# Optimization experiments

Measured on AMD Instinct MI355X. Metric: run time of the kernel, lower is better.

The kernel has to match this reference:

```python
import jax, jax.numpy as jnp
import numpy as np

CODEBOOK = 512
EMB_DIM = 64
COMMITMENT_COST = 0.25


def setup_inputs() -> dict:
    key = jax.random.key(0)
    k1, k2 = jax.random.split(key)
    inputs = jax.random.normal(k1, (32, EMB_DIM, 64, 64), dtype=jnp.float32)
    # nn.Embedding weight initialized uniform(-1/code_book_dim, 1/code_book_dim)
    embedding = jax.random.uniform(
        k2, (CODEBOOK, EMB_DIM), dtype=jnp.float32,
        minval=-1.0 / CODEBOOK, maxval=1.0 / CODEBOOK)
    return {"inputs": inputs, "embedding": embedding}


def reference(inputs, embedding):
    B, C, H, W = inputs.shape          # C == embedding_dim
    D = embedding.shape[1]
    x = jnp.transpose(inputs, (0, 2, 3, 1))      # [B,H,W,D] (permute(0,2,3,1))
    flat = x.reshape(-1, D)                       # [N,D]
    x2 = jnp.sum(flat * flat, axis=1, keepdims=True)          # [N,1]
    e2 = jnp.sum(embedding * embedding, axis=1)[None, :]       # [1,K]
    xe = flat @ embedding.T                                    # [N,K]
    distances = (x2 - 2.0 * xe + e2) / D                       # [N,K]
    encoding_indices = jnp.argmin(distances, axis=1)           # [N]
    quantized = embedding[encoding_indices].reshape(x.shape)   # [B,H,W,D]
    # MSE losses with detach semantics
    e_latent_loss = jnp.mean((jax.lax.stop_gradient(quantized) - x) ** 2)
    q_latent_loss = jnp.mean((quantized - jax.lax.stop_gradient(x)) ** 2)
    loss = q_latent_loss + COMMITMENT_COST * e_latent_loss
    # straight-through estimator (module default training=True)
    quantized_st = x + jax.lax.stop_gradient(quantized - x)
    out = jnp.transpose(quantized_st, (0, 3, 1, 2))            # back to NCHW
    indices = encoding_indices.reshape(B, -1)                  # [B, H*W]
    return loss, out, indices
```

## Files before the change

kernel.cpp:

```cpp
#include <hip/hip_runtime.h>


#define KCODE 512
#define EMB   64
#define HWSZ  4096
#define NPOS  131072
#define DELTA 2.5e-4f

typedef short short8  __attribute__((ext_vector_type(8)));
typedef float float4v __attribute__((ext_vector_type(4)));


__device__ __forceinline__ float np_sumsq64(const float* a) {
    #pragma clang fp contract(off)
    {
        float r0 = a[0] * a[0], r1 = a[1] * a[1], r2 = a[2] * a[2], r3 = a[3] * a[3];
        float r4 = a[4] * a[4], r5 = a[5] * a[5], r6 = a[6] * a[6], r7 = a[7] * a[7];
        for (int i = 8; i < 64; i += 8) {
            r0 += a[i + 0] * a[i + 0];
            r1 += a[i + 1] * a[i + 1];
            r2 += a[i + 2] * a[i + 2];
            r3 += a[i + 3] * a[i + 3];
            r4 += a[i + 4] * a[i + 4];
            r5 += a[i + 5] * a[i + 5];
            r6 += a[i + 6] * a[i + 6];
            r7 += a[i + 7] * a[i + 7];
        }
        return ((r0 + r1) + (r2 + r3)) + ((r4 + r5) + (r6 + r7));
    }
}

__device__ __forceinline__ float exact_u(const float* x, float x2,
                                         const float* ek, float e2k) {
    float t0 = 0.f, t1 = 0.f, t2 = 0.f, t3 = 0.f;
    #pragma unroll
    for (int c = 0; c < EMB; c += 4) {
        t0 = fmaf(x[c + 0], ek[c + 0], t0);
        t1 = fmaf(x[c + 1], ek[c + 1], t1);
        t2 = fmaf(x[c + 2], ek[c + 2], t2);
        t3 = fmaf(x[c + 3], ek[c + 3], t3);
    }
    float xe  = (t0 + t1) + (t2 + t3);
    float tmp = x2 - 2.0f * xe;
    return tmp + e2k;
}

__device__ __forceinline__ unsigned short bf16rne(float f) {
    unsigned u = __float_as_uint(f);
    unsigned r = (u + 0x7FFFu + ((u >> 16) & 1u)) >> 16;
    return (unsigned short)r;
}
__device__ __forceinline__ float bf16tof(unsigned short h) {
    return __uint_as_float((unsigned)h << 16);
}

#define INS(M1, I1, M2, I2, M3, v, i)                      \
    {                                                      \
        bool lt1 = (v) < (M1), lt2 = (v) < (M2), lt3 = (v) < (M3); \
        (M3) = lt2 ? (M2) : (lt3 ? (v) : (M3));            \
        (I2) = lt1 ? (I1) : (lt2 ? (i) : (I2));            \
        (M2) = lt1 ? (M1) : (lt2 ? (v) : (M2));            \
        (M1) = lt1 ? (v) : (M1);                           \
        (I1) = lt1 ? (i) : (I1);                           \
    }

__global__ void vq_prep(const float* __restrict__ emb, float* __restrict__ ws) {
    int f = blockIdx.x * blockDim.x + threadIdx.x;
    if (f == 0) { ((unsigned*)ws)[0] = 0u; ((unsigned*)ws)[1] = 0u; }
    if (f < KCODE) ws[520 + f] = np_sumsq64(emb + f * EMB);
    short8* bfrag = (short8*)(ws + 1032);
    int l = f & 63;
    int c = (f >> 6) & 1;
    int t = f >> 7;
    int code  = t * 16 + (l & 15);
    int dbase = 32 * c + ((l >> 4) & 3) * 8;
    const float* e = emb + code * EMB + dbase;
    short8 h, lo;
    #pragma unroll
    for (int j = 0; j < 8; ++j) {
        float v = e[j];
        unsigned short hb = bf16rne(v);
        float hf = bf16tof(hb);
        unsigned short lb = bf16rne(v - hf);
        h[j]  = (short)hb;
        lo[j] = (short)lb;
    }
    bfrag[t * 256 + c * 128 + 0 * 64 + l] = h;
    bfrag[t * 256 + c * 128 + 1 * 64 + l] = lo;
}

__global__ __launch_bounds__(256, 4) void vq_screen(
        const float*  __restrict__ in,
        const float*  __restrict__ e2np,
        const short8* __restrict__ bfrag,
        float*        __restrict__ out_idx,
        unsigned*     __restrict__ fullCnt,
        unsigned*     __restrict__ fullList,
        int fullCap) {
    const int tid  = threadIdx.x;
    const int wave = tid >> 6;
    const int lane = tid & 63;
    const int lg   = lane >> 4;
    const int lc   = lane & 15;
    const int wavePos = blockIdx.x * 64 + wave * 16;

    short8 fH[2], fL[2];
    {
        int pos = wavePos + lc;
        int b   = pos >> 12;
        int hw  = pos & (HWSZ - 1);
        const float* xb = in + ((size_t)b << 18) + hw;
        #pragma unroll
        for (int c = 0; c < 2; ++c) {
            short8 h, lo;
            #pragma unroll
            for (int j = 0; j < 8; ++j) {
                int d = 32 * c + lg * 8 + j;
                float g = -2.0f * xb[(size_t)d << 12];
                unsigned short hb = bf16rne(g);
                float hf = bf16tof(hb);
                unsigned short lb = bf16rne(g - hf);
                h[j]  = (short)hb;
                lo[j] = (short)lb;
            }
            fH[c] = h;
            fL[c] = lo;
        }
    }

    float m1[4], m2[4], m3[4];
    int   i1[4], i2[4];
    #pragma unroll
    for (int r = 0; r < 4; ++r) {
        m1[r] = 3.4e38f; m2[r] = 3.4e38f; m3[r] = 3.4e38f;
        i1[r] = 0;       i2[r] = 0;
    }

    short8 ceh0 = bfrag[lane],       cel0 = bfrag[64 + lane];
    short8 ceh1 = bfrag[128 + lane], cel1 = bfrag[192 + lane];
    float  ce2  = e2np[lc];
    #pragma unroll 2
    for (int t = 0; t < 32; ++t) {
        short8 neh0, nel0, neh1, nel1;
        float  ne2 = 0.0f;
        if (t < 31) {
            const short8* nb = bfrag + (t + 1) * 256;
            neh0 = nb[lane];       nel0 = nb[64 + lane];
            neh1 = nb[128 + lane]; nel1 = nb[192 + lane];
            ne2  = e2np[(t + 1) * 16 + lc];
        }
        const int kf = t * 16 + lc;
        float4v aH = {ce2, ce2, ce2, ce2};
        float4v aM = {0.f, 0.f, 0.f, 0.f};
        float4v aL = {0.f, 0.f, 0.f, 0.f};
        aH = __builtin_amdgcn_mfma_f32_16x16x32_bf16(fH[0], ceh0, aH, 0, 0, 0);
        aM = __builtin_amdgcn_mfma_f32_16x16x32_bf16(fH[0], cel0, aM, 0, 0, 0);
        aL = __builtin_amdgcn_mfma_f32_16x16x32_bf16(fL[0], ceh0, aL, 0, 0, 0);
        aH = __builtin_amdgcn_mfma_f32_16x16x32_bf16(fH[1], ceh1, aH, 0, 0, 0);
        aM = __builtin_amdgcn_mfma_f32_16x16x32_bf16(fH[1], cel1, aM, 0, 0, 0);
        aL = __builtin_amdgcn_mfma_f32_16x16x32_bf16(fL[1], ceh1, aL, 0, 0, 0);
        #pragma unroll
        for (int r = 0; r < 4; ++r) {
            float sv = (aH[r] + aM[r]) + aL[r];
            INS(m1[r], i1[r], m2[r], i2[r], m3[r], sv, kf);
        }
        ceh0 = neh0; cel0 = nel0; ceh1 = neh1; cel1 = nel1; ce2 = ne2;
    }

    #pragma unroll
    for (int r = 0; r < 4; ++r) {
        float M1 = m1[r], M2 = m2[r], M3 = m3[r];
        int   I1 = i1[r], I2 = i2[r];
        #pragma unroll
        for (int d = 1; d <= 8; d <<= 1) {
            float pm1 = __shfl_xor(M1, d, 64);
            int   pi1 = __shfl_xor(I1, d, 64);
            float pm2 = __shfl_xor(M2, d, 64);
            int   pi2 = __shfl_xor(I2, d, 64);
            float pm3 = __shfl_xor(M3, d, 64);
            INS(M1, I1, M2, I2, M3, pm1, pi1);
            INS(M1, I1, M2, I2, M3, pm2, pi2);
            M3 = fminf(M3, pm3);
        }
        m1[r] = M1; m2[r] = M2; m3[r] = M3;
        i1[r] = I1; i2[r] = I2;
    }

    if (lc == 0) {
        #pragma unroll
        for (int r = 0; r < 4; ++r) {
            int p  = wavePos + lg * 4 + r;
            int g2 = (m2[r] - m1[r] <= DELTA) ? 1 : 0;
            int g3 = (m3[r] - m1[r] <= DELTA) ? 1 : 0;
            int packed = i1[r] | (i2[r] << 9) | (g2 << 18) | (g3 << 19);
            out_idx[p] = (float)packed;
            if (g3) {
                unsigned slot = atomicAdd(fullCnt, 1u);
                if (slot < (unsigned)fullCap) fullList[slot] = (unsigned)p;
            }
        }
    }
}

__global__ __launch_bounds__(64) void vq_full(
        const float* __restrict__ in, const float* __restrict__ emb,
        const float* __restrict__ e2np, const unsigned* __restrict__ fullCnt,
        const unsigned* __restrict__ fullList, int fullCap,
        float* __restrict__ out_idx) {
    __shared__ float xbuf[EMB];
    const int lane = threadIdx.x;
    unsigned cnt = *fullCnt;
    if (cnt > (unsigned)fullCap) cnt = (unsigned)fullCap;

    for (unsigned idx = blockIdx.x; idx < cnt; idx += gridDim.x) {
        const int n  = (int)fullList[idx];
        const int b  = n >> 12;
        const int hw = n & (HWSZ - 1);
        xbuf[lane] = in[((size_t)b << 18) + ((size_t)lane << 12) + hw];
        __syncthreads();

        float x2;
        {
            #pragma clang fp contract(off)
            float r0 = xbuf[0] * xbuf[0], r1 = xbuf[1] * xbuf[1];
            float r2 = xbuf[2] * xbuf[2], r3 = xbuf[3] * xbuf[3];
            float r4 = xbuf[4] * xbuf[4], r5 = xbuf[5] * xbuf[5];
            float r6 = xbuf[6] * xbuf[6], r7 = xbuf[7] * xbuf[7];
            #pragma unroll 1
            for (int i = 8; i < EMB; i += 8) {
                r0 += xbuf[i + 0] * xbuf[i + 0];
                r1 += xbuf[i + 1] * xbuf[i + 1];
                r2 += xbuf[i + 2] * xbuf[i + 2];
                r3 += xbuf[i + 3] * xbuf[i + 3];
                r4 += xbuf[i + 4] * xbuf[i + 4];
                r5 += xbuf[i + 5] * xbuf[i + 5];
                r6 += xbuf[i + 6] * xbuf[i + 6];
                r7 += xbuf[i + 7] * xbuf[i + 7];
            }
            x2 = ((r0 + r1) + (r2 + r3)) + ((r4 + r5) + (r6 + r7));
        }

        float bu = 3.4e38f;
        int   bk = 0x7fffffff;
        #pragma unroll 1
        for (int j = 0; j < 8; ++j) {
            const int k = j * 64 + lane;
            const float* ek = emb + (size_t)k * EMB;
            float t0 = 0.f, t1 = 0.f, t2 = 0.f, t3 = 0.f;
            #pragma unroll 4
            for (int c = 0; c < EMB; c += 4) {
                t0 = fmaf(xbuf[c + 0], ek[c + 0], t0);
                t1 = fmaf(xbuf[c + 1], ek[c + 1], t1);
                t2 = fmaf(xbuf[c + 2], ek[c + 2], t2);
                t3 = fmaf(xbuf[c + 3], ek[c + 3], t3);
            }
            float xe  = (t0 + t1) + (t2 + t3);
            float tmp = x2 - 2.0f * xe;
            float u   = tmp + e2np[k];
            if (u < bu || (u == bu && k < bk)) { bu = u; bk = k; }
        }
        #pragma unroll
        for (int d = 1; d < 64; d <<= 1) {
            float ou = __shfl_xor(bu, d, 64);
            int   ok = __shfl_xor(bk, d, 64);
            if (ou < bu || (ou == bu && ok < bk)) { bu = ou; bk = ok; }
        }
        if (lane == 0) out_idx[n] = (float)bk;
        __syncthreads();
    }
}

__global__ __launch_bounds__(256) void vq_write(
        const float* __restrict__ in, const float* __restrict__ emb,
        const float* __restrict__ e2np,
        float* __restrict__ out_idx, float* __restrict__ out_q,
        float* __restrict__ partials,
        unsigned* __restrict__ ticket,
        float* __restrict__ out_loss) {
    const int tid = threadIdx.x;
    const int n   = blockIdx.x * 256 + tid;
    const int b   = n >> 12;
    const int hw  = n & (HWSZ - 1);

    const float* xp = in + ((size_t)b << 18) + hw;
    float x[EMB];
    #pragma unroll
    for (int c = 0; c < EMB; ++c) x[c] = xp[(size_t)c << 12];

    int v = (int)out_idx[n];
    int k = v & 511;
    int fl = v >> 18;
    if (fl) {
        float x2 = np_sumsq64(x);
        if (fl & 2) {
            float bu = 3.4e38f; int bk = 0;
            for (int kk = 0; kk < KCODE; ++kk) {
                float u = exact_u(x, x2, emb + kk * EMB, e2np[kk]);
                if (u < bu) { bu = u; bk = kk; }
            }
            k = bk;
        } else {
            int ia = v & 511, ib = (v >> 9) & 511;
            float u1 = exact_u(x, x2, emb + ia * EMB, e2np[ia]);
            float u2 = exact_u(x, x2, emb + ib * EMB, e2np[ib]);
            k = (u1 < u2) ? ia : (u2 < u1 ? ib : (ia < ib ? ia : ib));
        }
    }
    out_idx[n] = (float)k;

    const float4* qk = (const float4*)(emb + (size_t)k * EMB);
    float* op = out_q + ((size_t)b << 18) + hw;
    float s = 0.0f;
    #pragma unroll
    for (int c4 = 0; c4 < EMB / 4; ++c4) {
        float4 q = qk[c4];
        float d0 = q.x - x[c4 * 4 + 0];
        float d1 = q.y - x[c4 * 4 + 1];
        float d2 = q.z - x[c4 * 4 + 2];
        float d3 = q.w - x[c4 * 4 + 3];
        s = fmaf(d0, d0, s); s = fmaf(d1, d1, s);
        s = fmaf(d2, d2, s); s = fmaf(d3, d3, s);
        op[(size_t)(c4 * 4 + 0) << 12] = q.x;
        op[(size_t)(c4 * 4 + 1) << 12] = q.y;
        op[(size_t)(c4 * 4 + 2) << 12] = q.z;
        op[(size_t)(c4 * 4 + 3) << 12] = q.w;
    }

    #pragma unroll
    for (int off = 32; off > 0; off >>= 1)
        s += __shfl_down(s, off, 64);
    __shared__ float red[4];
    const int wave = tid >> 6;
    const int lane = tid & 63;
    if (lane == 0) red[wave] = s;
    __syncthreads();
    if (tid == 0) {
        partials[blockIdx.x] = (red[0] + red[1]) + (red[2] + red[3]);
        __threadfence();
        unsigned tk = atomicAdd(ticket, 1u);
        if (tk == 511u) {
            __threadfence();
            float a0 = 0.f, a1 = 0.f, a2 = 0.f, a3 = 0.f;
            float a4 = 0.f, a5 = 0.f, a6 = 0.f, a7 = 0.f;
            for (int i = 0; i < 512; i += 8) {
                a0 += partials[i + 0]; a1 += partials[i + 1];
                a2 += partials[i + 2]; a3 += partials[i + 3];
                a4 += partials[i + 4]; a5 += partials[i + 5];
                a6 += partials[i + 6]; a7 += partials[i + 7];
            }
            float tot = ((a0 + a1) + (a2 + a3)) + ((a4 + a5) + (a6 + a7));
            out_loss[0] = 1.25f * tot * (1.0f / ((float)NPOS * (float)EMB));
        }
    }
}

extern "C" void kernel_launch(void* const* d_in, const int* in_sizes, int n_in,
                              void* d_out, int out_size, void* d_ws, size_t ws_size,
                              hipStream_t stream) {
    const float* in  = (const float*)d_in[0];
    const float* emb = (const float*)d_in[1];
    float* ws  = (float*)d_ws;
    float* out = (float*)d_out;

    float*    out_loss = out;
    float*    out_q    = out + 1;
    float*    out_idx  = out + 1 + (size_t)NPOS * EMB;
    unsigned* fullCnt  = (unsigned*)ws;
    unsigned* ticket   = (unsigned*)ws + 1;
    float*    partials = ws + 8;
    float*    e2np     = ws + 520;
    short8*   bfrag    = (short8*)(ws + 1032);
    unsigned* fullList = (unsigned*)(ws + 33800);

    long avail = (long)(ws_size / 4) - 33800;
    int  fullCap = avail > 0 ? (avail > 1024 ? 1024 : (int)avail) : 0;

    vq_prep<<<16, 256, 0, stream>>>(emb, ws);
    vq_screen<<<NPOS / 64, 256, 0, stream>>>(in, e2np, bfrag, out_idx,
                                             fullCnt, fullList, fullCap);
    vq_full<<<256, 64, 0, stream>>>(in, emb, e2np, fullCnt, fullList, fullCap,
                                    out_idx);
    vq_write<<<NPOS / 256, 256, 0, stream>>>(in, emb, e2np, out_idx, out_q,
                                             partials, ticket, out_loss);
}
```

Measured before the change: 184.4 us.

## Split ambiguous-index resolution from quantized write; two threads per position in write

Moves the exact re-check of near-tie positions out of the write kernel into a separate vq_res2 kernel that exits early for unflagged positions. The write kernel becomes a lean streaming pass with two threads per position, each handling 32 channels, so it needs fewer registers and launches twice as many blocks. The screen kernel now stores plain indices for unambiguous positions. The cost is one extra kernel launch and a second read of out_idx, plus a workspace layout shift to make room for 1024 partial sums.

```diff
diff --git a/kernel.cpp b/kernel.cpp
--- a/kernel.cpp
+++ b/kernel.cpp
@@ -67,8 +67,8 @@
 __global__ void vq_prep(const float* __restrict__ emb, float* __restrict__ ws) {
     int f = blockIdx.x * blockDim.x + threadIdx.x;
     if (f == 0) { ((unsigned*)ws)[0] = 0u; ((unsigned*)ws)[1] = 0u; }
-    if (f < KCODE) ws[520 + f] = np_sumsq64(emb + f * EMB);
-    short8* bfrag = (short8*)(ws + 1032);
+    if (f < KCODE) ws[1032 + f] = np_sumsq64(emb + f * EMB);
+    short8* bfrag = (short8*)(ws + 1544);
     int l = f & 63;
     int c = (f >> 6) & 1;
     int t = f >> 7;
@@ -190,13 +190,18 @@
         #pragma unroll
         for (int r = 0; r < 4; ++r) {
             int p  = wavePos + lg * 4 + r;
-            int g2 = (m2[r] - m1[r] <= DELTA) ? 1 : 0;
-            int g3 = (m3[r] - m1[r] <= DELTA) ? 1 : 0;
-            int packed = i1[r] | (i2[r] << 9) | (g2 << 18) | (g3 << 19);
-            out_idx[p] = (float)packed;
-            if (g3) {
-                unsigned slot = atomicAdd(fullCnt, 1u);
-                if (slot < (unsigned)fullCap) fullList[slot] = (unsigned)p;
+            bool g2 = (m2[r] - m1[r] <= DELTA);
+            bool g3 = (m3[r] - m1[r] <= DELTA);
+            if (!g2 && !g3) {
+                out_idx[p] = (float)i1[r];
+            } else {
+                int packed = i1[r] | (i2[r] << 9)
+                           | (1 << 18) | (g3 ? (1 << 19) : 0);
+                out_idx[p] = (float)packed;
+                if (g3) {
+                    unsigned slot = atomicAdd(fullCnt, 1u);
+                    if (slot < (unsigned)fullCap) fullList[slot] = (unsigned)p;
+                }
             }
         }
     }
@@ -270,54 +275,67 @@
     }
 }
 
+__global__ __launch_bounds__(256) void vq_res2(
+        const float* __restrict__ in, const float* __restrict__ emb,
+        const float* __restrict__ e2np, float* __restrict__ out_idx) {
+    const int n = blockIdx.x * 256 + threadIdx.x;
+    const int v = (int)out_idx[n];
+    const int fl = v >> 18;
+    if (!fl) return;
+    const int b  = n >> 12;
+    const int hw = n & (HWSZ - 1);
+    const float* xp = in + ((size_t)b << 18) + hw;
+    float x[EMB];
+    #pragma unroll
+    for (int c = 0; c < EMB; ++c) x[c] = xp[(size_t)c << 12];
+    const float x2 = np_sumsq64(x);
+    int kk;
+    if (fl & 2) {
+        float bu = 3.4e38f; int bk = 0;
+        for (int k = 0; k < KCODE; ++k) {
+            float u = exact_u(x, x2, emb + k * EMB, e2np[k]);
+            if (u < bu) { bu = u; bk = k; }
+        }
+        kk = bk;
+    } else {
+        const int ia = v & 511, ib = (v >> 9) & 511;
+        float u1 = exact_u(x, x2, emb + (size_t)ia * EMB, e2np[ia]);
+        float u2 = exact_u(x, x2, emb + (size_t)ib * EMB, e2np[ib]);
+        kk = (u1 < u2) ? ia : (u2 < u1 ? ib : (ia < ib ? ia : ib));
+    }
+    out_idx[n] = (float)kk;
+}
+
 __global__ __launch_bounds__(256) void vq_write(
         const float* __restrict__ in, const float* __restrict__ emb,
-        const float* __restrict__ e2np,
-        float* __restrict__ out_idx, float* __restrict__ out_q,
+        const float* __restrict__ out_idx, float* __restrict__ out_q,
         float* __restrict__ partials,
         unsigned* __restrict__ ticket,
         float* __restrict__ out_loss) {
-    const int tid = threadIdx.x;
-    const int n   = blockIdx.x * 256 + tid;
-    const int b   = n >> 12;
-    const int hw  = n & (HWSZ - 1);
-
-    const float* xp = in + ((size_t)b << 18) + hw;
-    float x[EMB];
-    #pragma unroll
-    for (int c = 0; c < EMB; ++c) x[c] = xp[(size_t)c << 12];
-
-    int v = (int)out_idx[n];
-    int k = v & 511;
-    int fl = v >> 18;
-    if (fl) {
-        float x2 = np_sumsq64(x);
-        if (fl & 2) {
-            float bu = 3.4e38f; int bk = 0;
-            for (int kk = 0; kk < KCODE; ++kk) {
-                float u = exact_u(x, x2, emb + kk * EMB, e2np[kk]);
-                if (u < bu) { bu = u; bk = kk; }
-            }
-            k = bk;
-        } else {
-            int ia = v & 511, ib = (v >> 9) & 511;
-            float u1 = exact_u(x, x2, emb + ia * EMB, e2np[ia]);
-            float u2 = exact_u(x, x2, emb + ib * EMB, e2np[ib]);
-            k = (u1 < u2) ? ia : (u2 < u1 ? ib : (ia < ib ? ia : ib));
-        }
-    }
-    out_idx[n] = (float)k;
-
-    const float4* qk = (const float4*)(emb + (size_t)k * EMB);
-    float* op = out_q + ((size_t)b << 18) + hw;
+    const int tid  = threadIdx.x;
+    const int wave = tid >> 6;
+    const int lane = tid & 63;
+    const int g    = blockIdx.x * 256 + tid;
+    const int p    = g >> 1;
+    const int h    = g & 1;
+    const int b    = p >> 12;
+    const int hw   = p & (HWSZ - 1);
+
+    const int k = (int)out_idx[p];
+    const float4* q4 = (const float4*)(emb + (size_t)k * EMB + h * 32);
+    const size_t base = ((size_t)b << 18) + ((size_t)(h * 32) << 12) + hw;
+    const float* xp = in    + base;
+    float*       op = out_q + base;
+
     float s = 0.0f;
     #pragma unroll
-    for (int c4 = 0; c4 < EMB / 4; ++c4) {
-        float4 q = qk[c4];
-        float d0 = q.x - x[c4 * 4 + 0];
-        float d1 = q.y - x[c4 * 4 + 1];
-        float d2 = q.z - x[c4 * 4 + 2];
-        float d3 = q.w - x[c4 * 4 + 3];
+    for (int c4 = 0; c4 < 8; ++c4) {
+        float4 q = q4[c4];
+        float a0 = xp[(size_t)(c4 * 4 + 0) << 12];
+        float a1 = xp[(size_t)(c4 * 4 + 1) << 12];
+        float a2 = xp[(size_t)(c4 * 4 + 2) << 12];
+        float a3 = xp[(size_t)(c4 * 4 + 3) << 12];
+        float d0 = q.x - a0, d1 = q.y - a1, d2 = q.z - a2, d3 = q.w - a3;
         s = fmaf(d0, d0, s); s = fmaf(d1, d1, s);
         s = fmaf(d2, d2, s); s = fmaf(d3, d3, s);
         op[(size_t)(c4 * 4 + 0) << 12] = q.x;
@@ -330,19 +348,17 @@
     for (int off = 32; off > 0; off >>= 1)
         s += __shfl_down(s, off, 64);
     __shared__ float red[4];
-    const int wave = tid >> 6;
-    const int lane = tid & 63;
     if (lane == 0) red[wave] = s;
     __syncthreads();
     if (tid == 0) {
         partials[blockIdx.x] = (red[0] + red[1]) + (red[2] + red[3]);
         __threadfence();
         unsigned tk = atomicAdd(ticket, 1u);
-        if (tk == 511u) {
+        if (tk == 1023u) {
             __threadfence();
             float a0 = 0.f, a1 = 0.f, a2 = 0.f, a3 = 0.f;
             float a4 = 0.f, a5 = 0.f, a6 = 0.f, a7 = 0.f;
-            for (int i = 0; i < 512; i += 8) {
+            for (int i = 0; i < 1024; i += 8) {
                 a0 += partials[i + 0]; a1 += partials[i + 1];
                 a2 += partials[i + 2]; a3 += partials[i + 3];
                 a4 += partials[i + 4]; a5 += partials[i + 5];
@@ -368,11 +384,11 @@
     unsigned* fullCnt  = (unsigned*)ws;
     unsigned* ticket   = (unsigned*)ws + 1;
     float*    partials = ws + 8;
-    float*    e2np     = ws + 520;
-    short8*   bfrag    = (short8*)(ws + 1032);
-    unsigned* fullList = (unsigned*)(ws + 33800);
-
-    long avail = (long)(ws_size / 4) - 33800;
+    float*    e2np     = ws + 1032;
+    short8*   bfrag    = (short8*)(ws + 1544);
+    unsigned* fullList = (unsigned*)(ws + 34312);
+
+    long avail = (long)(ws_size / 4) - 34312;
     int  fullCap = avail > 0 ? (avail > 1024 ? 1024 : (int)avail) : 0;
 
     vq_prep<<<16, 256, 0, stream>>>(emb, ws);
@@ -380,6 +396,7 @@
                                              fullCnt, fullList, fullCap);
     vq_full<<<256, 64, 0, stream>>>(in, emb, e2np, fullCnt, fullList, fullCap,
                                     out_idx);
-    vq_write<<<NPOS / 256, 256, 0, stream>>>(in, emb, e2np, out_idx, out_q,
-                                             partials, ticket, out_loss);
-}
+    vq_res2<<<NPOS / 256, 256, 0, stream>>>(in, emb, e2np, out_idx);
+    vq_write<<<NPOS * 2 / 256, 256, 0, stream>>>(in, emb, out_idx, out_q,
+                                                 partials, ticket, out_loss);
+}
```

New measurement: 210.7 us. +14.3%, slower.
